# Performance work log

Measured on AMD Instinct MI355X. Metric: run time of the kernel, lower is better.

Reference implementation:

```python
import jax, jax.numpy as jnp
import numpy as np

N_CLASSES = 4
N_FEATURES = 13
N_HIDDEN = 13
N_STEPS = 100
FORGET_BIAS = 1.0


def setup_inputs() -> dict:
    key = jax.random.key(0)
    ks = jax.random.split(key, 10)
    B = 32768
    return {
        "x_input": jax.random.normal(ks[0], (B, N_STEPS, N_FEATURES), dtype=jnp.float32),
        # input projection (tf.random.normal mean=0.5 in original; values irrelevant for correctness test)
        "w_hidden": jax.random.normal(ks[1], (N_FEATURES, N_HIDDEN), dtype=jnp.float32) * 0.5 + 0.5,
        "b_hidden": jax.random.normal(ks[2], (N_HIDDEN,), dtype=jnp.float32) * 0.5 + 0.5,
        # BasicLSTMCell params: kernel [input_dim + hidden, 4*hidden], gate order (i, j, f, o)
        "lstm0_kernel": jax.random.normal(ks[3], (N_HIDDEN + N_HIDDEN, 4 * N_HIDDEN), dtype=jnp.float32) * 0.2,
        "lstm0_bias": jnp.zeros((4 * N_HIDDEN,), dtype=jnp.float32),
        "lstm1_kernel": jax.random.normal(ks[4], (N_HIDDEN + N_HIDDEN, 4 * N_HIDDEN), dtype=jnp.float32) * 0.2,
        "lstm1_bias": jnp.zeros((4 * N_HIDDEN,), dtype=jnp.float32),
        "w_output": jax.random.normal(ks[5], (N_HIDDEN, N_CLASSES), dtype=jnp.float32) * 0.5 + 0.5,
        "b_output": jax.random.normal(ks[6], (N_CLASSES,), dtype=jnp.float32) * 0.5 + 0.5,
    }


def _lstm_cell(x, c, h, kernel, bias):
    # BasicLSTMCell: z = [x; h] @ W + b, split -> i, j, f, o
    z = jnp.concatenate([x, h], axis=-1) @ kernel + bias
    i, j, f, o = jnp.split(z, 4, axis=-1)
    c_new = c * jax.nn.sigmoid(f + FORGET_BIAS) + jax.nn.sigmoid(i) * jnp.tanh(j)
    h_new = jnp.tanh(c_new) * jax.nn.sigmoid(o)
    return c_new, h_new


def reference(x_input, w_hidden, b_hidden, lstm0_kernel, lstm0_bias,
              lstm1_kernel, lstm1_bias, w_output, b_output):
    B = x_input.shape[0]
    # input projection + relu, batched over all timesteps: [B,T,F] -> [T,B,H]
    hidden = jax.nn.relu(jnp.einsum('btf,fh->bth', x_input, w_hidden) + b_hidden)
    hidden = jnp.transpose(hidden, (1, 0, 2))  # [T, B, H]

    zeros = jnp.zeros((B, N_HIDDEN), dtype=x_input.dtype)
    init = (zeros, zeros, zeros, zeros)  # (c0, h0, c1, h1)

    def step(carry, x_t):
        c0, h0, c1, h1 = carry
        c0, h0 = _lstm_cell(x_t, c0, h0, lstm0_kernel, lstm0_bias)
        c1, h1 = _lstm_cell(h0, c1, h1, lstm1_kernel, lstm1_bias)
        return (c0, h0, c1, h1), None

    (c0, h0, c1, h1), _ = jax.lax.scan(step, init, hidden)
    # last output of top LSTM layer -> output projection
    return h1 @ w_output + b_output
```

## Files before the change

kernel.cpp:

```cpp
#include <hip/hip_runtime.h>
#include <cstdint>

typedef __bf16          bf16x8 __attribute__((ext_vector_type(8)));
typedef float           f32x4  __attribute__((ext_vector_type(4)));
typedef unsigned short  u16x8  __attribute__((ext_vector_type(8)));
typedef unsigned int    u32x4  __attribute__((ext_vector_type(4)));

#define MFMA16(a,b,c) __builtin_amdgcn_mfma_f32_16x16x32_bf16((a),(b),(c),0,0,0)

__device__ __forceinline__ float rcpf(float x) { return __builtin_amdgcn_rcpf(x); }
__device__ __forceinline__ float ex2(float x)  { return __builtin_amdgcn_exp2f(x); }

__device__ __forceinline__ void split2(float v, unsigned short& hi, unsigned short& lo) {
    unsigned u = __builtin_bit_cast(unsigned, v);
    hi = (unsigned short)(u >> 16);
    float rem = v - __builtin_bit_cast(float, u & 0xffff0000u);
    lo = (unsigned short)(__builtin_bit_cast(unsigned, rem) >> 16);
}
__device__ __forceinline__ __bf16 bfbits(unsigned short b) { return __builtin_bit_cast(__bf16, b); }

__device__ __forceinline__ unsigned packhi2(float a, float b) {
    return __builtin_amdgcn_perm(__builtin_bit_cast(unsigned, b),
                                 __builtin_bit_cast(unsigned, a), 0x07060302u);
}
__device__ __forceinline__ float truncrem(float v) {
    return v - __builtin_bit_cast(float, __builtin_bit_cast(unsigned, v) & 0xffff0000u);
}


constexpr float SN1 = -1.4426950408889634f;
constexpr float SN2 = -2.8853900817779268f;
constexpr float C2  =  2.8853900817779268f;

__global__ __launch_bounds__(128, 4)
void lstm_fused(const float* __restrict__ x,
                const float* __restrict__ w_hidden,
                const float* __restrict__ b_hidden,
                const float* __restrict__ k0,
                const float* __restrict__ b0,
                const float* __restrict__ k1,
                const float* __restrict__ b1,
                const float* __restrict__ w_out,
                const float* __restrict__ b_out,
                float* __restrict__ out)
{
    __shared__ __attribute__((aligned(16))) unsigned short xh_s[2][2][384];
    __shared__ __attribute__((aligned(16))) unsigned short h0_s[2][2][384];
    __shared__ __attribute__((aligned(16))) unsigned short h1_s[2][384];

    const int lane = threadIdx.x & 63;
    const int role = threadIdx.x >> 6;
    const int col  = lane & 15;
    const int q    = lane >> 4;
    const int qh   = q & 1;
    const int s0   = blockIdx.x * 16;

    {
        unsigned short* a0 = &xh_s[0][0][0];
        unsigned short* a1 = &h0_s[0][0][0];
        for (int idx = threadIdx.x; idx < 1536; idx += 128) {
            unsigned short v = ((idx % 24) == 13 && ((idx / 384) & 1) == 0)
                             ? (unsigned short)0x3F80 : (unsigned short)0;
            a0[idx] = v; a1[idx] = v;
        }
        unsigned short* a2 = &h1_s[0][0];
        for (int idx = threadIdx.x; idx < 768; idx += 128) {
            unsigned short v = ((idx % 24) == 13 && ((idx / 384) & 1) == 0)
                             ? (unsigned short)0x3F80 : (unsigned short)0;
            a2[idx] = v;
        }
    }

    const float* kp = role ? k1 : k0;
    const float* bb = role ? b1 : b0;
    bf16x8 Kh[4], Kl[4];
    #pragma unroll
    for (int g = 0; g < 4; ++g) {
        const float sg = (g == 1) ? SN2 : SN1;
        bf16x8 hv{}, lv{};
        #pragma unroll
        for (int j = 0; j < 8; ++j) {
            int k = 8 * q + j;
            float w = 0.f;
            if (col < 13) {
                if (k < 13)                 w = kp[k * 52 + 13 * g + col];
                else if (k == 13)           w = bb[13 * g + col] + (g == 2 ? 1.f : 0.f);
                else if (k >= 16 && k < 29) w = kp[(13 + k - 16) * 52 + 13 * g + col];
            }
            w *= sg;
            unsigned short h_, l_;
            split2(w, h_, l_);
            hv[j] = bfbits(h_); lv[j] = bfbits(l_);
        }
        Kh[g] = hv; Kl[g] = lv;
    }

    bf16x8 Ph{}, Pl{};
    if (role) {
        #pragma unroll
        for (int j = 0; j < 8; ++j) {
            int k = 8 * q + j;
            float w = 0.f;
            if (col < 13) {
                if (k < 13)       w = w_hidden[k * 13 + col];
                else if (k == 13) w = b_hidden[col];
            }
            unsigned short h_, l_;
            split2(w, h_, l_);
            Ph[j] = bfbits(h_); Pl[j] = bfbits(l_);
        }
    }

    const float* xrow = x + (size_t)(s0 + col) * 1300;

    auto elem = [&](float zi, float zj, float zf, float zo, float& cs) -> float {
        float a   = ex2(zi);
        float b   = ex2(zj);
        float fe  = ex2(zf);
        float g   = ex2(zo);
        float opa = 1.f + a, opb = 1.f + b, opf = 1.f + fe;
        float pab = opa * opb;
        float r1  = rcpf(pab * opf);
        float tt  = fmaf(b, C2, -C2);
        float cn  = fmaf(cs, pab, tt * opf) * r1;
        cs = cn;
        float d   = ex2(cn);
        float r2  = rcpf((1.f + d) * (1.f + g));
        return (1.f - d) * r2;
    };

    auto cell = [&](const unsigned short* inH, const unsigned short* hidH,
                    unsigned short* outH, float* cst) {
        const unsigned short* pA = (q < 2) ? inH : hidH;
        bf16x8 ah = __builtin_bit_cast(bf16x8, *(const u16x8*)(pA + col * 24 + 8 * qh));
        bf16x8 al = __builtin_bit_cast(bf16x8, *(const u16x8*)(pA + 384 + col * 24 + 8 * qh));
        f32x4 z0 = {0.f,0.f,0.f,0.f}, z1 = z0, z2 = z0, z3 = z0;
        z0 = MFMA16(ah, Kh[0], z0); z0 = MFMA16(al, Kh[0], z0); z0 = MFMA16(ah, Kl[0], z0);
        z1 = MFMA16(ah, Kh[1], z1); z1 = MFMA16(al, Kh[1], z1); z1 = MFMA16(ah, Kl[1], z1);
        z2 = MFMA16(ah, Kh[2], z2); z2 = MFMA16(al, Kh[2], z2); z2 = MFMA16(ah, Kl[2], z2);
        z3 = MFMA16(ah, Kh[3], z3); z3 = MFMA16(al, Kh[3], z3); z3 = MFMA16(ah, Kl[3], z3);
        #pragma unroll
        for (int r = 0; r < 4; ++r) {
            float hv = elem(z0[r], z1[r], z2[r], z3[r], cst[r]);
            unsigned short hh, hl;
            split2(hv, hh, hl);
            if (col < 13) {
                outH[(4 * q + r) * 24 + col]       = hh;
                outH[384 + (4 * q + r) * 24 + col] = hl;
            }
        }
    };

    auto loadx = [&](int t, float* xv) {
        if (q < 2) {
            const float* p = xrow + t * 13 + 8 * q;
            const int lim = q ? 4 : 7;
            #pragma unroll
            for (int j = 0; j < 8; ++j) {
                int off = j > lim ? lim : j;
                xv[j] = p[off];
            }
        }
    };

    auto projc = [&](const float* xv, unsigned short* oH) {
        bf16x8 axh{}, axl{};
        if (q < 2) {
            unsigned hw0 = packhi2(xv[0], xv[1]);
            unsigned hw1 = packhi2(xv[2], xv[3]);
            unsigned hw2 = packhi2(xv[4], xv[5]);
            unsigned hw3 = packhi2(xv[6], xv[7]);
            unsigned lw0 = packhi2(truncrem(xv[0]), truncrem(xv[1]));
            unsigned lw1 = packhi2(truncrem(xv[2]), truncrem(xv[3]));
            unsigned lw2 = packhi2(truncrem(xv[4]), truncrem(xv[5]));
            unsigned lw3 = packhi2(truncrem(xv[6]), truncrem(xv[7]));
            if (q == 1) {
                hw2 = (hw2 & 0xffffu) | 0x3F800000u;
                lw2 &= 0xffffu;
                hw3 = 0u; lw3 = 0u;
            }
            u32x4 hv = {hw0, hw1, hw2, hw3};
            u32x4 lv = {lw0, lw1, lw2, lw3};
            axh = __builtin_bit_cast(bf16x8, hv);
            axl = __builtin_bit_cast(bf16x8, lv);
        }
        f32x4 zp = {0.f,0.f,0.f,0.f};
        zp = MFMA16(axh, Ph, zp);
        zp = MFMA16(axl, Ph, zp);
        zp = MFMA16(axh, Pl, zp);
        #pragma unroll
        for (int r = 0; r < 4; ++r) {
            float v = fmaxf(zp[r], 0.f);
            unsigned short hh, hl;
            split2(v, hh, hl);
            if (col < 13) {
                oH[(4 * q + r) * 24 + col]       = hh;
                oH[384 + (4 * q + r) * 24 + col] = hl;
            }
        }
    };

    float cst[4] = {0.f, 0.f, 0.f, 0.f};
    float xA[8], xB[8];

    if (role) loadx(0, xA);
    __syncthreads();
    if (role) { projc(xA, &xh_s[0][0][0]); loadx(1, xB); }
    __syncthreads();

    for (int i = 0; i < 100; i += 2) {
        if (role == 0) {
            cell(&xh_s[0][0][0], &h0_s[1][0][0], &h0_s[0][0][0], cst);
        } else {
            if (i < 98) loadx(i + 2, xA);
            if (i > 0)  cell(&h0_s[1][0][0], &h1_s[0][0], &h1_s[0][0], cst);
            projc(xB, &xh_s[1][0][0]);
        }
        __syncthreads();
        if (role == 0) {
            cell(&xh_s[1][0][0], &h0_s[0][0][0], &h0_s[1][0][0], cst);
        } else {
            if (i < 97) loadx(i + 3, xB);
            cell(&h0_s[0][0][0], &h1_s[0][0], &h1_s[0][0], cst);
            if (i < 98) projc(xA, &xh_s[0][0][0]);
        }
        __syncthreads();
    }

    if (role) {
        cell(&h0_s[1][0][0], &h1_s[0][0], &h1_s[0][0], cst);

        bf16x8 Oh{}, Ol{};
        #pragma unroll
        for (int j = 0; j < 8; ++j) {
            int k = 8 * q + j;
            float w = 0.f;
            if (col < 4) {
                if (k < 13)       w = w_out[k * 4 + col];
                else if (k == 13) w = b_out[col];
            }
            unsigned short h_, l_;
            split2(w, h_, l_);
            Oh[j] = bfbits(h_); Ol[j] = bfbits(l_);
        }
        const unsigned short* pA = &h1_s[0][0];
        bf16x8 ah = __builtin_bit_cast(bf16x8, *(const u16x8*)(pA + col * 24 + 8 * qh));
        bf16x8 al = __builtin_bit_cast(bf16x8, *(const u16x8*)(pA + 384 + col * 24 + 8 * qh));
        f32x4 zf = {0.f,0.f,0.f,0.f};
        zf = MFMA16(ah, Oh, zf);
        zf = MFMA16(al, Oh, zf);
        zf = MFMA16(ah, Ol, zf);
        if (col < 4) {
            #pragma unroll
            for (int r = 0; r < 4; ++r)
                out[(size_t)(s0 + 4 * q + r) * 4 + col] = zf[r];
        }
    }
}

extern "C" void kernel_launch(void* const* d_in, const int* in_sizes, int n_in,
                              void* d_out, int out_size, void* d_ws, size_t ws_size,
                              hipStream_t stream) {
    (void)in_sizes; (void)n_in; (void)d_ws; (void)ws_size; (void)out_size;
    lstm_fused<<<dim3(2048), dim3(128), 0, stream>>>(
        (const float*)d_in[0], (const float*)d_in[1], (const float*)d_in[2],
        (const float*)d_in[3], (const float*)d_in[4], (const float*)d_in[5],
        (const float*)d_in[6], (const float*)d_in[7], (const float*)d_in[8],
        (float*)d_out);
}
```

Baseline: 337.4 us.

## Process two timesteps per barrier phase in the pipelined LSTM loop

The loop now runs two LSTM timesteps per pipeline phase instead of one. The shared-memory input and layer-0 hidden ring buffers grow from two to four slots, and each wave runs its two cells back to back between barriers. This halves the number of __syncthreads calls in the 100-step recurrence, and with them the idle time the two waves spend waiting on each other. In exchange it doubles the staged x registers and the LDS footprint, and layer 1 now trails layer 0 by two timesteps, which could hurt occupancy or latency hiding.

```diff
diff --git a/kernel.cpp b/kernel.cpp
--- a/kernel.cpp
+++ b/kernel.cpp
@@ -44,8 +44,8 @@
                 const float* __restrict__ b_out,
                 float* __restrict__ out)
 {
-    __shared__ __attribute__((aligned(16))) unsigned short xh_s[2][2][384];
-    __shared__ __attribute__((aligned(16))) unsigned short h0_s[2][2][384];
+    __shared__ __attribute__((aligned(16))) unsigned short xh_s[4][2][384];
+    __shared__ __attribute__((aligned(16))) unsigned short h0_s[4][2][384];
     __shared__ __attribute__((aligned(16))) unsigned short h1_s[2][384];
 
     const int lane = threadIdx.x & 63;
@@ -58,7 +58,7 @@
     {
         unsigned short* a0 = &xh_s[0][0][0];
         unsigned short* a1 = &h0_s[0][0][0];
-        for (int idx = threadIdx.x; idx < 1536; idx += 128) {
+        for (int idx = threadIdx.x; idx < 3072; idx += 128) {
             unsigned short v = ((idx % 24) == 13 && ((idx / 384) & 1) == 0)
                              ? (unsigned short)0x3F80 : (unsigned short)0;
             a0[idx] = v; a1[idx] = v;
@@ -201,34 +201,50 @@
     };
 
     float cst[4] = {0.f, 0.f, 0.f, 0.f};
-    float xA[8], xB[8];
-
-    if (role) loadx(0, xA);
+    float xA0[8], xA1[8], xB0[8], xB1[8];
+
+    if (role) { loadx(0, xA0); loadx(1, xA1); }
     __syncthreads();
-    if (role) { projc(xA, &xh_s[0][0][0]); loadx(1, xB); }
+    if (role) {
+        projc(xA0, &xh_s[0][0][0]);
+        projc(xA1, &xh_s[1][0][0]);
+        loadx(2, xB0); loadx(3, xB1);
+    }
     __syncthreads();
 
-    for (int i = 0; i < 100; i += 2) {
+    for (int s = 0; s < 50; s += 2) {
         if (role == 0) {
-            cell(&xh_s[0][0][0], &h0_s[1][0][0], &h0_s[0][0][0], cst);
-        } else {
-            if (i < 98) loadx(i + 2, xA);
-            if (i > 0)  cell(&h0_s[1][0][0], &h1_s[0][0], &h1_s[0][0], cst);
-            projc(xB, &xh_s[1][0][0]);
-        }
-        __syncthreads();
-        if (role == 0) {
+            cell(&xh_s[0][0][0], &h0_s[3][0][0], &h0_s[0][0][0], cst);
             cell(&xh_s[1][0][0], &h0_s[0][0][0], &h0_s[1][0][0], cst);
         } else {
-            if (i < 97) loadx(i + 3, xB);
+            if (s < 48) { loadx(2 * s + 4, xA0); loadx(2 * s + 5, xA1); }
+            if (s > 0) {
+                cell(&h0_s[2][0][0], &h1_s[0][0], &h1_s[0][0], cst);
+                cell(&h0_s[3][0][0], &h1_s[0][0], &h1_s[0][0], cst);
+            }
+            projc(xB0, &xh_s[2][0][0]);
+            projc(xB1, &xh_s[3][0][0]);
+        }
+        __syncthreads();
+
+        if (role == 0) {
+            cell(&xh_s[2][0][0], &h0_s[1][0][0], &h0_s[2][0][0], cst);
+            cell(&xh_s[3][0][0], &h0_s[2][0][0], &h0_s[3][0][0], cst);
+        } else {
+            if (s < 47) { loadx(2 * s + 6, xB0); loadx(2 * s + 7, xB1); }
             cell(&h0_s[0][0][0], &h1_s[0][0], &h1_s[0][0], cst);
-            if (i < 98) projc(xA, &xh_s[0][0][0]);
+            cell(&h0_s[1][0][0], &h1_s[0][0], &h1_s[0][0], cst);
+            if (s < 48) {
+                projc(xA0, &xh_s[0][0][0]);
+                projc(xA1, &xh_s[1][0][0]);
+            }
         }
         __syncthreads();
     }
 
     if (role) {
-        cell(&h0_s[1][0][0], &h1_s[0][0], &h1_s[0][0], cst);
+        cell(&h0_s[2][0][0], &h1_s[0][0], &h1_s[0][0], cst);
+        cell(&h0_s[3][0][0], &h1_s[0][0], &h1_s[0][0], cst);
 
         bf16x8 Oh{}, Ol{};
         #pragma unroll
```

Measured after the change: 374.9 us. 1.11x slower.
